# Kernel tuning notes

Measured on AMD Instinct MI355X. Metric: run time of the kernel, lower is better.

The kernel has to match this reference:

```python
import jax, jax.numpy as jnp
import numpy as np

D = 1024          # d_model
DQ = D // 4       # embedding dim (d_model//4)
DH = D // 2       # head hidden (d_model//2)
P = 6             # n_digit_positions = max_int_digits + n_decimal_digits
NOPS, NPT = 9, 10
B, T = 8, 2048


def _ln(x, g, b, eps=1e-5):
    m = jnp.mean(x, axis=-1, keepdims=True)
    v = jnp.mean(jnp.square(x - m), axis=-1, keepdims=True)
    return (x - m) * jax.lax.rsqrt(v + eps) * g + b


def _xavier(key, shape):
    fan_in, fan_out = shape[-2], shape[-1]
    lim = np.sqrt(6.0 / (fan_in + fan_out))
    return jax.random.uniform(key, shape, jnp.float32, -lim, lim)


def setup_inputs() -> dict:
    key = jax.random.key(0)
    ks = jax.random.split(key, 20)
    inp = {
        'hidden': jax.random.normal(ks[0], (B, T, D), jnp.float32),
        'operation_type': jax.random.randint(ks[1], (B,), 0, NOPS),
        'param_type': jax.random.randint(ks[2], (B, T), 0, NPT),
        # embeddings (std=0.02 like the torch init)
        'op_embed': 0.02 * jax.random.normal(ks[3], (NOPS, DQ), jnp.float32),
        'pt_embed': 0.02 * jax.random.normal(ks[4], (NPT, DQ), jnp.float32),
        'pos_embed': 0.02 * jax.random.normal(ks[5], (P, DQ), jnp.float32),
        # context_proj: Linear(D + D//2 -> D) + LayerNorm(D)
        'ctx_w': _xavier(ks[6], (D + D // 2, D)),
        'ctx_b': jnp.zeros((D,), jnp.float32),
        'ctx_g': jnp.ones((D,), jnp.float32),
        'ctx_beta': jnp.zeros((D,), jnp.float32),
        # sign_head: Linear(D->DH), LN(DH), Linear(DH->3)
        'sign_w1': _xavier(ks[7], (D, DH)),
        'sign_b1': jnp.zeros((DH,), jnp.float32),
        'sign_g': jnp.ones((DH,), jnp.float32),
        'sign_beta': jnp.zeros((DH,), jnp.float32),
        'sign_w2': _xavier(ks[8], (DH, 3)),
        'sign_b2': jnp.zeros((3,), jnp.float32),
        # digit heads stacked over positions: Linear(D+DQ->DH), LN(DH), Linear(DH->10)
        'dig_w1': _xavier(ks[9], (P, D + DQ, DH)),
        'dig_b1': jnp.zeros((P, DH), jnp.float32),
        'dig_g': jnp.ones((P, DH), jnp.float32),
        'dig_beta': jnp.zeros((P, DH), jnp.float32),
        'dig_w2': _xavier(ks[10], (P, DH, 10)),
        'dig_b2': jnp.zeros((P, 10), jnp.float32),
        'aux_w1': _xavier(ks[11], (D, DH)),
        'aux_b1': jnp.zeros((DH,), jnp.float32),
        'aux_w2': _xavier(ks[12], (DH, 1)),
        'aux_b2': jnp.zeros((1,), jnp.float32),
    }
    return inp


def reference(hidden, operation_type, param_type, op_embed, pt_embed, pos_embed,
              ctx_w, ctx_b, ctx_g, ctx_beta,
              sign_w1, sign_b1, sign_g, sign_beta, sign_w2, sign_b2,
              dig_w1, dig_b1, dig_g, dig_beta, dig_w2, dig_b2,
              aux_w1, aux_b1, aux_w2, aux_b2):
    b, t, d = hidden.shape
    gelu = lambda x: jax.nn.gelu(x, approximate=False)  # torch nn.GELU default

    op_emb = jnp.broadcast_to(op_embed[operation_type][:, None, :], (b, t, DQ))
    pm_emb = pt_embed[param_type]                       # [B,T,DQ]
    ctx_in = jnp.concatenate([hidden, op_emb, pm_emb], axis=-1)  # [B,T,1.5D]
    context = gelu(_ln(ctx_in @ ctx_w + ctx_b, ctx_g, ctx_beta))  # [B,T,D]

    sh = gelu(_ln(context @ sign_w1 + sign_b1, sign_g, sign_beta))
    sign_logits = sh @ sign_w2 + sign_b2                # [B,T,3]

    # digit heads, vectorized over position. concat(context, pos_emb[p]) @ W1
    # == context @ W1[:, :D] + pos_emb[p] @ W1[:, D:]
    h = (jnp.einsum('btd,pdh->btph', context, dig_w1[:, :D, :])
         + jnp.einsum('pq,pqh->ph', pos_embed, dig_w1[:, D:, :])
         + dig_b1)                                      # [B,T,P,DH]
    h = gelu(_ln(h, dig_g, dig_beta))
    digit_logits = jnp.einsum('btph,pho->btpo', h, dig_w2) + dig_b2  # [B,T,P,10]

    aux_value = gelu(context @ aux_w1 + aux_b1) @ aux_w2 + aux_b2    # [B,T,1]

    return sign_logits, digit_logits, aux_value
```

## Files before the change

### kernel.cpp

```cpp
#include <hip/hip_runtime.h>
#include <hip/hip_bf16.h>

typedef unsigned short u16;
typedef __attribute__((ext_vector_type(8))) __bf16 bf16x8;
typedef __attribute__((ext_vector_type(4))) float f32x4;

typedef __attribute__((address_space(1))) const void GVoid;
typedef __attribute__((address_space(3))) void LVoid;

__device__ __forceinline__ void async_load16(const u16* g, u16* l) {
    __builtin_amdgcn_global_load_lds((GVoid*)g, (LVoid*)l, 16, 0, 0);
}

__device__ __forceinline__ float bf2f(u16 u) {
    union { unsigned i; float f; } v; v.i = ((unsigned)u) << 16; return v.f;
}
__device__ __forceinline__ u16 f2bf(float f) {
    union { float f; unsigned i; } v; v.f = f;
    unsigned r = (v.i + 0x7FFFu + ((v.i >> 16) & 1u)) >> 16;
    return (u16)r;
}
__device__ __forceinline__ float gelu_f(float x) {
    float t = x * fmaf(0.0356774081f, x * x, 0.7978845608f);
    float e = __expf(2.0f * t);
    float r = 1.0f / (e + 1.0f);
    return x - x * r;
}

#define OP_E   0
#define PT_E   2304
#define POS_E  4864
#define CTX_B  6400
#define CTX_G  7424
#define CTX_BE 8448
#define S_B1   9472
#define S_G    9984
#define S_BE   10496
#define S_B2   11008
#define D_G    11012
#define D_BE   14084
#define D_B2   17156
#define A_B1   17216
#define A_B2   17728

struct SmallTab {
    const float* src[15];
    int off[15];
    int cnt[15];
};

__global__ __launch_bounds__(256) void convert_small(SmallTab tab, u16* __restrict__ dst)
{
    int idx = blockIdx.x * 256 + threadIdx.x;
#pragma unroll
    for (int e = 0; e < 15; ++e) {
        if (idx < tab.cnt[e]) {
            dst[tab.off[e] + idx] = f2bf(tab.src[e][idx]);
            return;
        }
        idx -= tab.cnt[e];
    }
}

__global__ __launch_bounds__(256) void transpose_all(
    const float* __restrict__ ctx_w, const float* __restrict__ sign_w1,
    const float* __restrict__ aux_w1, const float* __restrict__ dig_w1,
    u16* __restrict__ ctxWt, u16* __restrict__ BtAll)
{
    __shared__ u16 tl[32][33];
    int z = blockIdx.z;
    const float* src; u16* dst; size_t srcOff = 0; int srcLd, cols;
    if (z == 8) { src = ctx_w; dst = ctxWt; srcLd = 1024; cols = 1024; }
    else {
        srcLd = 512; cols = 512;
        if (z == 0) src = sign_w1;
        else if (z == 1) src = aux_w1;
        else { src = dig_w1; srcOff = (size_t)(z - 2) * 1280 * 512; }
        dst = BtAll + (size_t)z * 512 * 1024;
    }
    int n0 = blockIdx.x * 32;
    if (n0 >= cols) return;
    int k0 = blockIdx.y * 32;
    int t = threadIdx.x;
    int r = t >> 3;
    int c4 = (t & 7) * 4;
    float4 v = *(const float4*)&src[srcOff + (size_t)(k0 + r) * srcLd + n0 + c4];
    tl[r][c4 + 0] = f2bf(v.x); tl[r][c4 + 1] = f2bf(v.y);
    tl[r][c4 + 2] = f2bf(v.z); tl[r][c4 + 3] = f2bf(v.w);
    __syncthreads();
    ushort4 o;
    o.x = tl[c4 + 0][r]; o.y = tl[c4 + 1][r]; o.z = tl[c4 + 2][r]; o.w = tl[c4 + 3][r];
    *(ushort4*)&dst[(size_t)(n0 + r) * 1024 + k0 + c4] = o;
}

__global__ __launch_bounds__(256) void precompute_bias(
    const float* __restrict__ ctx_w, const float* __restrict__ dig_w1,
    const float* __restrict__ op_embed, const float* __restrict__ pt_embed,
    const float* __restrict__ pos_embed, const float* __restrict__ dig_b1,
    const int* __restrict__ op_type,
    float* __restrict__ E_op, float* __restrict__ P_pt, float* __restrict__ dbias)
{
    int idx = blockIdx.x * 256 + threadIdx.x;
    if (idx < 8192) {
        int b = idx >> 10, n = idx & 1023;
        const float* e = op_embed + op_type[b] * 256;
        float s = 0.f;
        for (int q = 0; q < 256; ++q)
            s += e[q] * ctx_w[(size_t)(1024 + q) * 1024 + n];
        E_op[idx] = s;
    } else if (idx < 18432) {
        int i = idx - 8192;
        int v = i >> 10, n = i & 1023;
        const float* e = pt_embed + v * 256;
        float s = 0.f;
        for (int q = 0; q < 256; ++q)
            s += e[q] * ctx_w[(size_t)(1280 + q) * 1024 + n];
        P_pt[i] = s;
    } else if (idx < 21504) {
        int i = idx - 18432;
        int p = i >> 9, h = i & 511;
        const float* e = pos_embed + p * 256;
        float s = dig_b1[p * 512 + h];
        for (int q = 0; q < 256; ++q)
            s += e[q] * dig_w1[(size_t)p * 1280 * 512 + (size_t)(1024 + q) * 512 + h];
        dbias[i] = s;
    }
}

__global__ __launch_bounds__(256) void build_vec(
    const u16* __restrict__ csm, const float* __restrict__ dbias,
    float* __restrict__ biasAll, float* __restrict__ gammaAll,
    float* __restrict__ betaAll)
{
    int n = blockIdx.x * 256 + threadIdx.x;
    float bi, g, be;
    if (n < 512) {
        bi = bf2f(csm[S_B1 + n]); g = bf2f(csm[S_G + n]); be = bf2f(csm[S_BE + n]);
    } else if (n < 1024) {
        bi = bf2f(csm[A_B1 + n - 512]); g = 1.f; be = 0.f;
    } else {
        int h = n - 1024;
        bi = dbias[h]; g = bf2f(csm[D_G + h]); be = bf2f(csm[D_BE + h]);
    }
    biasAll[n] = bi; gammaAll[n] = g; betaAll[n] = be;
}

__global__ __launch_bounds__(256) void build_w2pad(
    const float* __restrict__ sign_w2, const float* __restrict__ dig_w2,
    const float* __restrict__ aux_w2, u16* __restrict__ W2pad)
{
    int idx = blockIdx.x * 256 + threadIdx.x;
    int row = idx >> 12, k = idx & 4095;
    int r = row >> 4, o = row & 15;
    float v = 0.f;
    if (r == 0) {
        if (o < 3 && k < 512) v = sign_w2[k * 3 + o];
    } else if (r == 7) {
        if (o == 0 && k >= 512 && k < 1024) v = aux_w2[k - 512];
    } else {
        int p = r - 1, lo = 1024 + p * 512;
        if (o < 10 && k >= lo && k < lo + 512) v = dig_w2[(size_t)p * 5120 + (k - lo) * 10 + o];
    }
    W2pad[idx] = f2bf(v);
}

__global__ __launch_bounds__(256) void gemm_bf16(
    const u16* __restrict__ A, const u16* __restrict__ Bt, u16* __restrict__ C,
    int M, int N, int K)
{
    __shared__ u16 As[128 * 32];
    __shared__ u16 Bs[128 * 32];
    const int tid = threadIdx.x;
    const int wid = tid >> 6, lane = tid & 63;
    const int m0 = blockIdx.x * 128, n0 = blockIdx.y * 128;
    const int mw = (wid >> 1) * 64, nw = (wid & 1) * 64;
    const int quad = lane >> 4, r16 = lane & 15;

    f32x4 acc[4][4] = {};

    const int srow = wid * 32 + (lane >> 2);
    const int scol = (lane & 3) * 8;
    const u16* gA = A + (size_t)(m0 + srow) * K + scol;
    const u16* gB = Bt + (size_t)(n0 + srow) * K + scol;
    u16* lA = As + wid * 32 * 32;
    u16* lB = Bs + wid * 32 * 32;

    for (int k0 = 0; k0 < K; k0 += 32) {
        async_load16(gA + k0, lA);
        async_load16(gA + k0 + (size_t)16 * K, lA + 16 * 32);
        async_load16(gB + k0, lB);
        async_load16(gB + k0 + (size_t)16 * K, lB + 16 * 32);
        __syncthreads();
        bf16x8 af[4], bw[4];
#pragma unroll
        for (int i = 0; i < 4; ++i)
            af[i] = *(const bf16x8*)&As[(mw + i * 16 + r16) * 32 + quad * 8];
#pragma unroll
        for (int j = 0; j < 4; ++j)
            bw[j] = *(const bf16x8*)&Bs[(nw + j * 16 + r16) * 32 + quad * 8];
#pragma unroll
        for (int i = 0; i < 4; ++i)
#pragma unroll
            for (int j = 0; j < 4; ++j)
                acc[i][j] = __builtin_amdgcn_mfma_f32_16x16x32_bf16(
                    af[i], bw[j], acc[i][j], 0, 0, 0);
        __syncthreads();
    }

#pragma unroll
    for (int i = 0; i < 4; ++i) {
#pragma unroll
        for (int j = 0; j < 4; ++j) {
            int col = n0 + nw + j * 16 + r16;
            size_t base = (size_t)(m0 + mw + i * 16 + quad * 4) * N + col;
#pragma unroll
            for (int r = 0; r < 4; ++r)
                C[base + (size_t)r * N] = f2bf(acc[i][j][r]);
        }
    }
}

__global__ __launch_bounds__(256) void gemm_f32a(
    const float* __restrict__ A, const u16* __restrict__ Bt, u16* __restrict__ C,
    int M, int N, int K)
{
    __shared__ u16 As[128 * 32];
    __shared__ u16 Bs[128 * 32];
    const int tid = threadIdx.x;
    const int wid = tid >> 6, lane = tid & 63;
    const int m0 = blockIdx.x * 128, n0 = blockIdx.y * 128;
    const int mw = (wid >> 1) * 64, nw = (wid & 1) * 64;
    const int quad = lane >> 4, r16 = lane & 15;

    f32x4 acc[4][4] = {};

    const int srow = wid * 32 + (lane >> 2);
    const int scol = (lane & 3) * 8;
    const u16* gB = Bt + (size_t)(n0 + srow) * K + scol;
    u16* lB = Bs + wid * 32 * 32;

    const int r0 = tid >> 2;
    const int c8 = (tid & 3) * 8;

    for (int k0 = 0; k0 < K; k0 += 32) {
        async_load16(gB + k0, lB);
        async_load16(gB + k0 + (size_t)16 * K, lB + 16 * 32);
        const float* p0 = &A[(size_t)(m0 + r0) * K + k0 + c8];
        const float* p1 = &A[(size_t)(m0 + 64 + r0) * K + k0 + c8];
        float4 x = *(const float4*)p0, y = *(const float4*)(p0 + 4);
        float4 u = *(const float4*)p1, w = *(const float4*)(p1 + 4);
        uint4 a0, a1;
        a0.x = f2bf(x.x) | ((unsigned)f2bf(x.y) << 16);
        a0.y = f2bf(x.z) | ((unsigned)f2bf(x.w) << 16);
        a0.z = f2bf(y.x) | ((unsigned)f2bf(y.y) << 16);
        a0.w = f2bf(y.z) | ((unsigned)f2bf(y.w) << 16);
        a1.x = f2bf(u.x) | ((unsigned)f2bf(u.y) << 16);
        a1.y = f2bf(u.z) | ((unsigned)f2bf(u.w) << 16);
        a1.z = f2bf(w.x) | ((unsigned)f2bf(w.y) << 16);
        a1.w = f2bf(w.z) | ((unsigned)f2bf(w.w) << 16);
        *(uint4*)&As[r0 * 32 + c8] = a0;
        *(uint4*)&As[(64 + r0) * 32 + c8] = a1;
        __syncthreads();

        bf16x8 af[4], bw[4];
#pragma unroll
        for (int i = 0; i < 4; ++i)
            af[i] = *(const bf16x8*)&As[(mw + i * 16 + r16) * 32 + quad * 8];
#pragma unroll
        for (int j = 0; j < 4; ++j)
            bw[j] = *(const bf16x8*)&Bs[(nw + j * 16 + r16) * 32 + quad * 8];
#pragma unroll
        for (int i = 0; i < 4; ++i)
#pragma unroll
            for (int j = 0; j < 4; ++j)
                acc[i][j] = __builtin_amdgcn_mfma_f32_16x16x32_bf16(
                    af[i], bw[j], acc[i][j], 0, 0, 0);
        __syncthreads();
    }

#pragma unroll
    for (int i = 0; i < 4; ++i) {
#pragma unroll
        for (int j = 0; j < 4; ++j) {
            int col = n0 + nw + j * 16 + r16;
            size_t base = (size_t)(m0 + mw + i * 16 + quad * 4) * N + col;
#pragma unroll
            for (int r = 0; r < 4; ++r)
                C[base + (size_t)r * N] = f2bf(acc[i][j][r]);
        }
    }
}

__global__ __launch_bounds__(256) void ln_ctx_kernel(
    const u16* __restrict__ pre, const float* __restrict__ E_op,
    const float* __restrict__ P_pt, const int* __restrict__ ptype,
    const u16* __restrict__ csm, u16* __restrict__ ctx, int tokOff)
{
    __shared__ float red[8];
    int local = blockIdx.x;
    int token = tokOff + local;
    int b = token >> 11;
    int pt = ptype[token];
    int tid = threadIdx.x;
    int c = tid * 4;
    int wid = tid >> 6, lane = tid & 63;

    ushort4 xp = *(const ushort4*)&pre[(size_t)local * 1024 + c];
    float4 eo = *(const float4*)&E_op[b * 1024 + c];
    float4 pp = *(const float4*)&P_pt[pt * 1024 + c];
    ushort4 cb4 = *(const ushort4*)&csm[CTX_B + c];
    float x[4];
    x[0] = bf2f(xp.x) + eo.x + pp.x + bf2f(cb4.x);
    x[1] = bf2f(xp.y) + eo.y + pp.y + bf2f(cb4.y);
    x[2] = bf2f(xp.z) + eo.z + pp.z + bf2f(cb4.z);
    x[3] = bf2f(xp.w) + eo.w + pp.w + bf2f(cb4.w);

    float s = x[0] + x[1] + x[2] + x[3];
    float s2 = x[0]*x[0] + x[1]*x[1] + x[2]*x[2] + x[3]*x[3];
    for (int off = 32; off; off >>= 1) { s += __shfl_xor(s, off); s2 += __shfl_xor(s2, off); }
    if (lane == 0) { red[wid] = s; red[4 + wid] = s2; }
    __syncthreads();
    s  = red[0] + red[1] + red[2] + red[3];
    s2 = red[4] + red[5] + red[6] + red[7];
    float mean = s * (1.f / 1024.f);
    float var = fmaxf(s2 * (1.f / 1024.f) - mean * mean, 0.f);
    float rs = rsqrtf(var + 1e-5f);

    ushort4 g4 = *(const ushort4*)&csm[CTX_G + c];
    ushort4 b4 = *(const ushort4*)&csm[CTX_BE + c];
    ushort4 o;
    o.x = f2bf(gelu_f((x[0] - mean) * rs * bf2f(g4.x) + bf2f(b4.x)));
    o.y = f2bf(gelu_f((x[1] - mean) * rs * bf2f(g4.y) + bf2f(b4.y)));
    o.z = f2bf(gelu_f((x[2] - mean) * rs * bf2f(g4.z) + bf2f(b4.z)));
    o.w = f2bf(gelu_f((x[3] - mean) * rs * bf2f(g4.w) + bf2f(b4.w)));
    *(ushort4*)&ctx[(size_t)token * 1024 + c] = o;
}

__global__ __launch_bounds__(256) void ln_stats(
    const u16* __restrict__ hp, const float* __restrict__ biasAll,
    float2* __restrict__ stats, int Rh)
{
    int wid = threadIdx.x >> 6, lane = threadIdx.x & 63;
    int idx = blockIdx.x * 4 + wid;
    int token = idx >> 3, s = idx & 7;
    const u16* row = hp + (size_t)token * 4096 + s * 512 + lane * 8;
    ushort4 a = ((const ushort4*)row)[0];
    ushort4 b = ((const ushort4*)row)[1];
    u16 xr[8]; *(ushort4*)&xr[0] = a; *(ushort4*)&xr[4] = b;
    const float* bi = biasAll + s * 512 + lane * 8;
    float4 b0 = *(const float4*)bi, b1 = *(const float4*)(bi + 4);
    float bb[8] = {b0.x, b0.y, b0.z, b0.w, b1.x, b1.y, b1.z, b1.w};
    float sm = 0.f, s2 = 0.f;
#pragma unroll
    for (int j = 0; j < 8; ++j) {
        float v = bf2f(xr[j]) + bb[j];
        sm += v; s2 += v * v;
    }
    for (int off = 32; off; off >>= 1) { sm += __shfl_xor(sm, off); s2 += __shfl_xor(s2, off); }
    if (lane == 0) {
        float mean = sm * (1.f / 512.f);
        float var = fmaxf(s2 * (1.f / 512.f) - mean * mean, 0.f);
        float2 st = make_float2(mean, rsqrtf(var + 1e-5f));
        if (s == 1) st = make_float2(0.f, 1.f);
        stats[idx] = st;
    }
}

__global__ __launch_bounds__(256) void gemm_final(
    const u16* __restrict__ A, const u16* __restrict__ W2pad,
    const float* __restrict__ biasAll, const float* __restrict__ gammaAll,
    const float* __restrict__ betaAll, const float2* __restrict__ stats,
    float* __restrict__ out_pre, int Rh)
{
    __shared__ u16 As[128 * 32];
    __shared__ u16 Bs[128 * 32];
    const int tid = threadIdx.x;
    const int wid = tid >> 6, lane = tid & 63;
    const int m0 = blockIdx.x * 128;
    const int ks = blockIdx.y, kbase = ks * 1024;
    const int mw = (wid >> 1) * 64, nw = (wid & 1) * 64;
    const int quad = lane >> 4, r16 = lane & 15;

    f32x4 acc[4][4] = {};

    const int srow = wid * 32 + (lane >> 2);
    const int scol = (lane & 3) * 8;
    const u16* gB = W2pad + (size_t)srow * 4096 + kbase + scol;
    u16* lB = Bs + wid * 32 * 32;

    const int r0 = tid >> 2;
    const int c8 = (tid & 3) * 8;

    for (int k0 = 0; k0 < 1024; k0 += 32) {
        async_load16(gB + k0, lB);
        async_load16(gB + k0 + (size_t)16 * 4096, lB + 16 * 32);
        int kk = kbase + k0 + c8;
        int sl = kk >> 9;
        float4 bi0 = *(const float4*)&biasAll[kk], bi1 = *(const float4*)&biasAll[kk + 4];
        float4 g0 = *(const float4*)&gammaAll[kk], g1 = *(const float4*)&gammaAll[kk + 4];
        float4 be0 = *(const float4*)&betaAll[kk], be1 = *(const float4*)&betaAll[kk + 4];
        float bb[8] = {bi0.x, bi0.y, bi0.z, bi0.w, bi1.x, bi1.y, bi1.z, bi1.w};
        float gg[8] = {g0.x, g0.y, g0.z, g0.w, g1.x, g1.y, g1.z, g1.w};
        float bt[8] = {be0.x, be0.y, be0.z, be0.w, be1.x, be1.y, be1.z, be1.w};
#pragma unroll
        for (int h = 0; h < 2; ++h) {
            int row = m0 + r0 + h * 64;
            const u16* ap = A + (size_t)row * 4096 + kk;
            ushort4 xa = ((const ushort4*)ap)[0];
            ushort4 xb = ((const ushort4*)ap)[1];
            u16 xr[8]; *(ushort4*)&xr[0] = xa; *(ushort4*)&xr[4] = xb;
            float2 st = stats[row * 8 + sl];
            u16 o[8];
#pragma unroll
            for (int j = 0; j < 8; ++j) {
                float v = (bf2f(xr[j]) + bb[j] - st.x) * st.y * gg[j] + bt[j];
                o[j] = f2bf(gelu_f(v));
            }
            *(uint4*)&As[(h * 64 + r0) * 32 + c8] = *(const uint4*)&o[0];
        }
        __syncthreads();

        bf16x8 af[4], bw[4];
#pragma unroll
        for (int i = 0; i < 4; ++i)
            af[i] = *(const bf16x8*)&As[(mw + i * 16 + r16) * 32 + quad * 8];
#pragma unroll
        for (int j = 0; j < 4; ++j)
            bw[j] = *(const bf16x8*)&Bs[(nw + j * 16 + r16) * 32 + quad * 8];
#pragma unroll
        for (int i = 0; i < 4; ++i)
#pragma unroll
            for (int j = 0; j < 4; ++j)
                acc[i][j] = __builtin_amdgcn_mfma_f32_16x16x32_bf16(
                    af[i], bw[j], acc[i][j], 0, 0, 0);
        __syncthreads();
    }

    float* op = out_pre + (size_t)ks * Rh * 128;
#pragma unroll
    for (int i = 0; i < 4; ++i) {
#pragma unroll
        for (int j = 0; j < 4; ++j) {
            int col = nw + j * 16 + r16;
            size_t base = (size_t)(m0 + mw + i * 16 + quad * 4) * 128 + col;
#pragma unroll
            for (int r = 0; r < 4; ++r)
                op[base + (size_t)r * 128] = acc[i][j][r];
        }
    }
}

__global__ __launch_bounds__(256) void gather_out(
    const float* __restrict__ out_pre, const u16* __restrict__ csm,
    float* __restrict__ out, int tokOff, int Rh)
{
    int idx = blockIdx.x * 256 + threadIdx.x;
    if (idx >= Rh * 64) return;
    int local = idx >> 6;
    int c = idx & 63;
    int token = tokOff + local;
    size_t P = (size_t)Rh * 128;
    size_t base = (size_t)local * 128;
    int col;
    if (c < 3) col = c;
    else if (c == 63) col = 7 * 16;
    else { int d = c - 3; int p = d / 10; col = (p + 1) * 16 + (d - p * 10); }
    float v = out_pre[base + col] + out_pre[P + base + col]
            + out_pre[2 * P + base + col] + out_pre[3 * P + base + col];
    if (c < 3) {
        out[(size_t)token * 3 + c] = v + bf2f(csm[S_B2 + c]);
    } else if (c == 63) {
        out[1032192 + (size_t)token] = v + bf2f(csm[A_B2]);
    } else {
        int d = c - 3;
        int p = d / 10, o = d - p * 10;
        out[49152 + ((size_t)token * 6 + p) * 10 + o] = v + bf2f(csm[D_B2 + p * 10 + o]);
    }
}

extern "C" void kernel_launch(void* const* d_in, const int* in_sizes, int n_in,
                              void* d_out, int out_size, void* d_ws, size_t ws_size,
                              hipStream_t stream) {
    const float* hidden    = (const float*)d_in[0];
    const int*   op_type   = (const int*)d_in[1];
    const int*   pt_type   = (const int*)d_in[2];
    const float* op_embed  = (const float*)d_in[3];
    const float* pt_embed  = (const float*)d_in[4];
    const float* pos_embed = (const float*)d_in[5];
    const float* ctx_w     = (const float*)d_in[6];
    const float* sign_w1   = (const float*)d_in[10];
    const float* sign_w2   = (const float*)d_in[14];
    const float* dig_w1    = (const float*)d_in[16];
    const float* dig_b1    = (const float*)d_in[17];
    const float* dig_w2    = (const float*)d_in[20];
    const float* aux_w1    = (const float*)d_in[22];
    const float* aux_w2    = (const float*)d_in[24];

    char* ws = (char*)d_ws;
    u16*    ctxWt    = (u16*)(ws + 0);
    u16*    BtAll    = (u16*)(ws + 2097152);
    float*  E_op     = (float*)(ws + 10485760);
    float*  P_pt     = (float*)(ws + 10518528);
    float*  dbias    = (float*)(ws + 10559488);
    u16*    csm      = (u16*)(ws + 10571776);
    float*  biasAll  = (float*)(ws + 10637312);
    float*  gammaAll = (float*)(ws + 10653696);
    float*  betaAll  = (float*)(ws + 10670080);
    float2* stats    = (float2*)(ws + 10686464);
    u16*    context  = (u16*)(ws + 11735040);
    u16*    scratch  = (u16*)(ws + 45289472);
    u16*    W2pad    = ctxWt;
    size_t S = (ws_size > 45289472) ? ws_size - 45289472 : 0;

    int Rc = 16384;
    while ((size_t)Rc * 2048 > S && Rc > 128) Rc >>= 1;
    int Rh = 16384;
    while ((size_t)Rh * 8192 > S && Rh > 128) Rh >>= 1;

    float* out = (float*)d_out;

    SmallTab tab;
    const float* srcs[15] = { op_embed, pt_embed, pos_embed,
                              (const float*)d_in[7], (const float*)d_in[8], (const float*)d_in[9],
                              (const float*)d_in[11], (const float*)d_in[12], (const float*)d_in[13],
                              (const float*)d_in[15],
                              (const float*)d_in[18], (const float*)d_in[19], (const float*)d_in[21],
                              (const float*)d_in[23], (const float*)d_in[25] };
    const int offs[15] = { OP_E, PT_E, POS_E, CTX_B, CTX_G, CTX_BE,
                           S_B1, S_G, S_BE, S_B2,
                           D_G, D_BE, D_B2, A_B1, A_B2 };
    const int cnts[15] = { 2304, 2560, 1536, 1024, 1024, 1024,
                           512, 512, 512, 3,
                           3072, 3072, 60, 512, 1 };
    for (int i = 0; i < 15; ++i) { tab.src[i] = srcs[i]; tab.off[i] = offs[i]; tab.cnt[i] = cnts[i]; }
    convert_small<<<70, 256, 0, stream>>>(tab, csm);

    transpose_all<<<dim3(32, 32, 9), 256, 0, stream>>>(
        ctx_w, sign_w1, aux_w1, dig_w1, ctxWt, BtAll);
    precompute_bias<<<84, 256, 0, stream>>>(
        ctx_w, dig_w1, op_embed, pt_embed, pos_embed, dig_b1, op_type,
        E_op, P_pt, dbias);
    build_vec<<<16, 256, 0, stream>>>(csm, dbias, biasAll, gammaAll, betaAll);

    for (int t0 = 0; t0 < 16384; t0 += Rc) {
        gemm_f32a<<<dim3(Rc / 128, 8), 256, 0, stream>>>(
            hidden + (size_t)t0 * 1024, ctxWt, scratch, Rc, 1024, 1024);
        ln_ctx_kernel<<<Rc, 256, 0, stream>>>(
            scratch, E_op, P_pt, pt_type, csm, context, t0);
    }

    build_w2pad<<<2048, 256, 0, stream>>>(sign_w2, dig_w2, aux_w2, W2pad);

    for (int t0 = 0; t0 < 16384; t0 += Rh) {
        gemm_bf16<<<dim3(Rh / 128, 32), 256, 0, stream>>>(
            context + (size_t)t0 * 1024, BtAll, scratch, Rh, 4096, 1024);
        ln_stats<<<Rh * 2, 256, 0, stream>>>(scratch, biasAll, stats, Rh);
        float* out_pre = (float*)(context + (size_t)t0 * 1024);
        gemm_final<<<dim3(Rh / 128, 4), 256, 0, stream>>>(
            scratch, W2pad, biasAll, gammaAll, betaAll, stats, out_pre, Rh);
        gather_out<<<(Rh * 64 + 255) / 256, 256, 0, stream>>>(
            out_pre, csm, out, t0, Rh);
    }
}
```

Baseline: 564.5 us.

## Fuse LayerNorm statistics into head GEMM epilogue and swizzle LDS tiles

The separate ln_stats pass, which re-read the bf16 hidden activations, is removed. The head GEMM epilogue now computes per-row partial sums and sums of squares, reduces them across lanes and adds them into a zeroed stats buffer with atomics; a small finalize kernel then converts them to mean and rstd. Separately, all three GEMMs XOR-swizzle the LDS column offsets to cut bank conflicts on the fragment reads. The cost is two extra small launches, atomic traffic, and a float sum order that is no longer deterministic.

```diff
diff --git a/kernel.cpp b/kernel.cpp
--- a/kernel.cpp
+++ b/kernel.cpp
@@ -164,9 +164,29 @@
     W2pad[idx] = f2bf(v);
 }
 
+__global__ __launch_bounds__(256) void zero_stats(float2* __restrict__ st, int n)
+{
+    int idx = blockIdx.x * 256 + threadIdx.x;
+    if (idx < n) st[idx] = make_float2(0.f, 0.f);
+}
+
+__global__ __launch_bounds__(256) void finalize_stats(float2* __restrict__ st, int n)
+{
+    int idx = blockIdx.x * 256 + threadIdx.x;
+    if (idx >= n) return;
+    int s = idx & 7;
+    float2 a = st[idx];
+    float mean = a.x * (1.f / 512.f);
+    float var = fmaxf(a.y * (1.f / 512.f) - mean * mean, 0.f);
+    float2 o = make_float2(mean, rsqrtf(var + 1e-5f));
+    if (s == 1) o = make_float2(0.f, 1.f);
+    st[idx] = o;
+}
+
 __global__ __launch_bounds__(256) void gemm_bf16(
     const u16* __restrict__ A, const u16* __restrict__ Bt, u16* __restrict__ C,
-    int M, int N, int K)
+    int M, int N, int K,
+    const float* __restrict__ biasAll, float2* __restrict__ statsAcc)
 {
     __shared__ u16 As[128 * 32];
     __shared__ u16 Bs[128 * 32];
@@ -179,11 +199,12 @@
     f32x4 acc[4][4] = {};
 
     const int srow = wid * 32 + (lane >> 2);
-    const int scol = (lane & 3) * 8;
+    const int scol = (((lane & 3) ^ ((lane >> 3) & 3)) * 8);
     const u16* gA = A + (size_t)(m0 + srow) * K + scol;
     const u16* gB = Bt + (size_t)(n0 + srow) * K + scol;
     u16* lA = As + wid * 32 * 32;
     u16* lB = Bs + wid * 32 * 32;
+    const int rsw = ((r16 >> 1) & 3) * 8;
 
     for (int k0 = 0; k0 < K; k0 += 32) {
         async_load16(gA + k0, lA);
@@ -194,10 +215,10 @@
         bf16x8 af[4], bw[4];
 #pragma unroll
         for (int i = 0; i < 4; ++i)
-            af[i] = *(const bf16x8*)&As[(mw + i * 16 + r16) * 32 + quad * 8];
+            af[i] = *(const bf16x8*)&As[(mw + i * 16 + r16) * 32 + (quad * 8 ^ rsw)];
 #pragma unroll
         for (int j = 0; j < 4; ++j)
-            bw[j] = *(const bf16x8*)&Bs[(nw + j * 16 + r16) * 32 + quad * 8];
+            bw[j] = *(const bf16x8*)&Bs[(nw + j * 16 + r16) * 32 + (quad * 8 ^ rsw)];
 #pragma unroll
         for (int i = 0; i < 4; ++i)
 #pragma unroll
@@ -216,6 +237,34 @@
 #pragma unroll
             for (int r = 0; r < 4; ++r)
                 C[base + (size_t)r * N] = f2bf(acc[i][j][r]);
+        }
+    }
+
+    int sl = n0 >> 9;
+    if (statsAcc != nullptr && sl != 1) {
+        float b4[4];
+#pragma unroll
+        for (int j = 0; j < 4; ++j) b4[j] = biasAll[n0 + nw + j * 16 + r16];
+#pragma unroll
+        for (int i = 0; i < 4; ++i) {
+#pragma unroll
+            for (int r = 0; r < 4; ++r) {
+                float s = 0.f, s2 = 0.f;
+#pragma unroll
+                for (int j = 0; j < 4; ++j) {
+                    float v = acc[i][j][r] + b4[j];
+                    s += v; s2 += v * v;
+                }
+                for (int off = 1; off < 16; off <<= 1) {
+                    s += __shfl_xor(s, off); s2 += __shfl_xor(s2, off);
+                }
+                if (r16 == 0) {
+                    int row = m0 + mw + i * 16 + quad * 4 + r;
+                    float* sa = (float*)&statsAcc[row * 8 + sl];
+                    atomicAdd(sa, s);
+                    atomicAdd(sa + 1, s2);
+                }
+            }
         }
     }
 }
@@ -235,12 +284,14 @@
     f32x4 acc[4][4] = {};
 
     const int srow = wid * 32 + (lane >> 2);
-    const int scol = (lane & 3) * 8;
+    const int scol = (((lane & 3) ^ ((lane >> 3) & 3)) * 8);
     const u16* gB = Bt + (size_t)(n0 + srow) * K + scol;
     u16* lB = Bs + wid * 32 * 32;
+    const int rsw = ((r16 >> 1) & 3) * 8;
 
     const int r0 = tid >> 2;
     const int c8 = (tid & 3) * 8;
+    const int c8s = (((tid & 3) ^ ((tid >> 3) & 3)) * 8);
 
     for (int k0 = 0; k0 < K; k0 += 32) {
         async_load16(gB + k0, lB);
@@ -258,17 +309,17 @@
         a1.y = f2bf(u.z) | ((unsigned)f2bf(u.w) << 16);
         a1.z = f2bf(w.x) | ((unsigned)f2bf(w.y) << 16);
         a1.w = f2bf(w.z) | ((unsigned)f2bf(w.w) << 16);
-        *(uint4*)&As[r0 * 32 + c8] = a0;
-        *(uint4*)&As[(64 + r0) * 32 + c8] = a1;
+        *(uint4*)&As[r0 * 32 + c8s] = a0;
+        *(uint4*)&As[(64 + r0) * 32 + c8s] = a1;
         __syncthreads();
 
         bf16x8 af[4], bw[4];
 #pragma unroll
         for (int i = 0; i < 4; ++i)
-            af[i] = *(const bf16x8*)&As[(mw + i * 16 + r16) * 32 + quad * 8];
+            af[i] = *(const bf16x8*)&As[(mw + i * 16 + r16) * 32 + (quad * 8 ^ rsw)];
 #pragma unroll
         for (int j = 0; j < 4; ++j)
-            bw[j] = *(const bf16x8*)&Bs[(nw + j * 16 + r16) * 32 + quad * 8];
+            bw[j] = *(const bf16x8*)&Bs[(nw + j * 16 + r16) * 32 + (quad * 8 ^ rsw)];
 #pragma unroll
         for (int i = 0; i < 4; ++i)
 #pragma unroll
@@ -336,36 +387,6 @@
     *(ushort4*)&ctx[(size_t)token * 1024 + c] = o;
 }
 
-__global__ __launch_bounds__(256) void ln_stats(
-    const u16* __restrict__ hp, const float* __restrict__ biasAll,
-    float2* __restrict__ stats, int Rh)
-{
-    int wid = threadIdx.x >> 6, lane = threadIdx.x & 63;
-    int idx = blockIdx.x * 4 + wid;
-    int token = idx >> 3, s = idx & 7;
-    const u16* row = hp + (size_t)token * 4096 + s * 512 + lane * 8;
-    ushort4 a = ((const ushort4*)row)[0];
-    ushort4 b = ((const ushort4*)row)[1];
-    u16 xr[8]; *(ushort4*)&xr[0] = a; *(ushort4*)&xr[4] = b;
-    const float* bi = biasAll + s * 512 + lane * 8;
-    float4 b0 = *(const float4*)bi, b1 = *(const float4*)(bi + 4);
-    float bb[8] = {b0.x, b0.y, b0.z, b0.w, b1.x, b1.y, b1.z, b1.w};
-    float sm = 0.f, s2 = 0.f;
-#pragma unroll
-    for (int j = 0; j < 8; ++j) {
-        float v = bf2f(xr[j]) + bb[j];
-        sm += v; s2 += v * v;
-    }
-    for (int off = 32; off; off >>= 1) { sm += __shfl_xor(sm, off); s2 += __shfl_xor(s2, off); }
-    if (lane == 0) {
-        float mean = sm * (1.f / 512.f);
-        float var = fmaxf(s2 * (1.f / 512.f) - mean * mean, 0.f);
-        float2 st = make_float2(mean, rsqrtf(var + 1e-5f));
-        if (s == 1) st = make_float2(0.f, 1.f);
-        stats[idx] = st;
-    }
-}
-
 __global__ __launch_bounds__(256) void gemm_final(
     const u16* __restrict__ A, const u16* __restrict__ W2pad,
     const float* __restrict__ biasAll, const float* __restrict__ gammaAll,
@@ -384,12 +405,14 @@
     f32x4 acc[4][4] = {};
 
     const int srow = wid * 32 + (lane >> 2);
-    const int scol = (lane & 3) * 8;
+    const int scol = (((lane & 3) ^ ((lane >> 3) & 3)) * 8);
     const u16* gB = W2pad + (size_t)srow * 4096 + kbase + scol;
     u16* lB = Bs + wid * 32 * 32;
+    const int rsw = ((r16 >> 1) & 3) * 8;
 
     const int r0 = tid >> 2;
     const int c8 = (tid & 3) * 8;
+    const int c8s = (((tid & 3) ^ ((tid >> 3) & 3)) * 8);
 
     for (int k0 = 0; k0 < 1024; k0 += 32) {
         async_load16(gB + k0, lB);
@@ -416,17 +439,17 @@
                 float v = (bf2f(xr[j]) + bb[j] - st.x) * st.y * gg[j] + bt[j];
                 o[j] = f2bf(gelu_f(v));
             }
-            *(uint4*)&As[(h * 64 + r0) * 32 + c8] = *(const uint4*)&o[0];
+            *(uint4*)&As[(h * 64 + r0) * 32 + c8s] = *(const uint4*)&o[0];
         }
         __syncthreads();
 
         bf16x8 af[4], bw[4];
 #pragma unroll
         for (int i = 0; i < 4; ++i)
-            af[i] = *(const bf16x8*)&As[(mw + i * 16 + r16) * 32 + quad * 8];
+            af[i] = *(const bf16x8*)&As[(mw + i * 16 + r16) * 32 + (quad * 8 ^ rsw)];
 #pragma unroll
         for (int j = 0; j < 4; ++j)
-            bw[j] = *(const bf16x8*)&Bs[(nw + j * 16 + r16) * 32 + quad * 8];
+            bw[j] = *(const bf16x8*)&Bs[(nw + j * 16 + r16) * 32 + (quad * 8 ^ rsw)];
 #pragma unroll
         for (int i = 0; i < 4; ++i)
 #pragma unroll
@@ -552,9 +575,12 @@
     build_w2pad<<<2048, 256, 0, stream>>>(sign_w2, dig_w2, aux_w2, W2pad);
 
     for (int t0 = 0; t0 < 16384; t0 += Rh) {
+        int nst = Rh * 8;
+        zero_stats<<<(nst + 255) / 256, 256, 0, stream>>>(stats, nst);
         gemm_bf16<<<dim3(Rh / 128, 32), 256, 0, stream>>>(
-            context + (size_t)t0 * 1024, BtAll, scratch, Rh, 4096, 1024);
-        ln_stats<<<Rh * 2, 256, 0, stream>>>(scratch, biasAll, stats, Rh);
+            context + (size_t)t0 * 1024, BtAll, scratch, Rh, 4096, 1024,
+            biasAll, stats);
+        finalize_stats<<<(nst + 255) / 256, 256, 0, stream>>>(stats, nst);
         float* out_pre = (float*)(context + (size_t)t0 * 1024);
         gemm_final<<<dim3(Rh / 128, 4), 256, 0, stream>>>(
             scratch, W2pad, biasAll, gammaAll, betaAll, stats, out_pre, Rh);
```

Result: slower. 595.5 us (+5.5%).
